# Kernel tuning notes

Measured on AMD Instinct MI355X. Metric: run time of the kernel, lower is better.

Reference implementation:

```python
import jax, jax.numpy as jnp
import numpy as np

B, S, E, H, T = 2, 1024, 1024, 16, 32
D = E // H  # head_dim = 64
EPS = 1e-12
SCALE = float(np.sqrt(T) / np.sqrt(D))  # sqrt(num_templates) * 1/sqrt(head_dim)


def _apply_rope(q, k):
    # q, k: [B, S, H, D] float32 (source casts to float for RoPE)
    d = q.shape[-1]
    s = q.shape[1]
    inv_freq = 1.0 / (10000.0 ** (jnp.arange(0, d, 2, dtype=jnp.float32) / d))
    ang = jnp.arange(s, dtype=jnp.float32)[:, None] * inv_freq[None, :]  # [S, D/2]
    cis = jnp.exp(1j * ang)[None, :, None, :]  # [1, S, 1, D/2] complex64

    def rot(v):
        vc = v.reshape(v.shape[:-1] + (d // 2, 2))
        vc = jax.lax.complex(vc[..., 0], vc[..., 1]) * cis
        return jnp.stack([jnp.real(vc), jnp.imag(vc)], axis=-1).reshape(v.shape)

    return rot(q), rot(k)


def _l2norm(v):
    # F.normalize(v, dim=-1): v / max(||v||, eps)
    n = jnp.sqrt(jnp.sum(v * v, axis=-1, keepdims=True))
    return v / jnp.maximum(n, EPS)


def _forward(x, Wq, Wk, Wv, Wo, templates, bind_proj):
    b, s, e = x.shape
    h, d = H, D
    q = (x @ Wq.T).reshape(b, s, h, d)
    k = (x @ Wk.T).reshape(b, s, h, d)
    v = (x @ Wv.T).reshape(b, s, h, d)
    q, k = _apply_rope(q, k)
    q = q.transpose(0, 2, 1, 3)  # [B,H,S,D]
    k = k.transpose(0, 2, 1, 3)
    v = v.transpose(0, 2, 1, 3)

    tpl = _l2norm(templates)  # [H,T,D]
    # forward rfft uses norm='ortho' in the source
    q_freq = jnp.fft.rfft(q, axis=-1, norm='ortho')  # [B,H,S,F], F=D//2+1
    k_freq = jnp.fft.rfft(k, axis=-1, norm='ortho')
    t_conj = jnp.conj(jnp.fft.rfft(tpl, axis=-1, norm='ortho'))[None, :, None, :, :]  # [1,H,1,T,F]

    # NOTE: irfft in the source uses the DEFAULT 'backward' norm (asymmetric with
    # the ortho rfft) -- reproduce that exactly.
    q_bind = jnp.fft.irfft(q_freq[:, :, :, None, :] * t_conj, n=d, axis=-1)  # [B,H,S,T,D]
    k_bind = jnp.fft.irfft(k_freq[:, :, :, None, :] * t_conj, n=d, axis=-1)

    proj = bind_proj[None, :, None, None, :]  # [1,H,1,1,D]
    q_sig = _l2norm(jnp.sum(q_bind * proj, axis=-1))  # [B,H,S,T]
    k_sig = _l2norm(jnp.sum(k_bind * proj, axis=-1))

    scores = jnp.einsum('bhqt,bhkt->bhqk', q_sig, k_sig) * SCALE  # [B,H,S,S]
    attn = jax.nn.softmax(scores, axis=-1)  # dropout is identity in eval mode
    out = jnp.einsum('bhqk,bhkd->bqhd', attn, v).reshape(b, s, e)
    return out @ Wo.T


def setup_inputs() -> dict:
    key = jax.random.key(0)
    ks = jax.random.split(key, 7)
    lim = 1.0 / np.sqrt(E)
    x = jax.random.normal(ks[0], (B, S, E), jnp.float32)
    Wq = jax.random.uniform(ks[1], (E, E), jnp.float32, -lim, lim)
    Wk = jax.random.uniform(ks[2], (E, E), jnp.float32, -lim, lim)
    Wv = jax.random.uniform(ks[3], (E, E), jnp.float32, -lim, lim)
    Wo = jax.random.uniform(ks[4], (E, E), jnp.float32, -lim, lim)
    templates = jax.random.normal(ks[5], (H, T, D), jnp.float32)
    bind_proj = jax.random.normal(ks[6], (H, D), jnp.float32) * 0.02
    return {"x": x, "Wq": Wq, "Wk": Wk, "Wv": Wv, "Wo": Wo,
            "templates": templates, "bind_proj": bind_proj}


def reference(x, Wq, Wk, Wv, Wo, templates, bind_proj):
    return _forward(x, Wq, Wk, Wv, Wo, templates, bind_proj)
```

## Files before the change

kernel.cpp:

```cpp
#include <hip/hip_runtime.h>
#include <math.h>

#define S_ 1024
#define T_ 32
#define SCALE_F 0.7071067811865476f

typedef unsigned int uint;
typedef unsigned short ushort;
typedef __bf16 bf16x8 __attribute__((ext_vector_type(8)));
typedef float f32x16 __attribute__((ext_vector_type(16)));

union FragU { uint4 q; bf16x8 v; };

#define MFMA(a, b, c) __builtin_amdgcn_mfma_f32_32x32x16_bf16((a), (b), (c), 0, 0, 0)

__device__ __forceinline__ uint rne16(float f) {
  uint u = __builtin_bit_cast(uint, f);
  u += 0x7fffu + ((u >> 16) & 1u);
  return u >> 16;
}

__device__ __forceinline__ void split8a(const float* f, uint4& hi, uint4& lo) {
  uint h[8], m[8];
#pragma unroll
  for (int i = 0; i < 8; ++i) {
    uint u = __builtin_bit_cast(uint, f[i]);
    h[i] = u >> 16;
    float fh = __builtin_bit_cast(float, u & 0xffff0000u);
    m[i] = __builtin_bit_cast(uint, f[i] - fh) >> 16;
  }
  hi = make_uint4(h[0] | (h[1] << 16), h[2] | (h[3] << 16),
                  h[4] | (h[5] << 16), h[6] | (h[7] << 16));
  lo = make_uint4(m[0] | (m[1] << 16), m[2] | (m[3] << 16),
                  m[4] | (m[5] << 16), m[6] | (m[7] << 16));
}

__device__ __forceinline__ uint4 rne8(const float4& A, const float4& B) {
  float f[8] = {A.x, A.y, A.z, A.w, B.x, B.y, B.z, B.w};
  uint h[8];
#pragma unroll
  for (int i = 0; i < 8; ++i) h[i] = rne16(f[i]);
  return make_uint4(h[0] | (h[1] << 16), h[2] | (h[3] << 16),
                    h[4] | (h[5] << 16), h[6] | (h[7] << 16));
}

__global__ __launch_bounds__(256) void k_cvtall(
    const float* __restrict__ X, const float* __restrict__ Wq,
    const float* __restrict__ Wk, const float* __restrict__ Wv,
    const float* __restrict__ Wo, ushort* __restrict__ Xb,
    ushort* __restrict__ Wqb, ushort* __restrict__ Wkb,
    ushort* __restrict__ Wvb, ushort* __restrict__ Wob) {
  int i = blockIdx.x * 256 + threadIdx.x;
  const float* src;
  ushort* dst;
  int j;
  if (i < 262144)      { src = X;  dst = Xb;  j = i; }
  else if (i < 393216) { src = Wq; dst = Wqb; j = i - 262144; }
  else if (i < 524288) { src = Wk; dst = Wkb; j = i - 393216; }
  else if (i < 655360) { src = Wv; dst = Wvb; j = i - 524288; }
  else                 { src = Wo; dst = Wob; j = i - 655360; }
  float4 a = *reinterpret_cast<const float4*>(src + j * 8);
  float4 b = *reinterpret_cast<const float4*>(src + j * 8 + 4);
  *reinterpret_cast<uint4*>(dst + j * 8) = rne8(a, b);
}

__global__ __launch_bounds__(64) void k_cs(float* __restrict__ cs) {
  int s = blockIdx.x * 2 + (threadIdx.x >> 5);
  int p = threadIdx.x & 31;
  float invf = powf(10000.0f, (-2.0f * p) / 64.0f);
  float sn, c;
  sincosf((float)s * invf, &sn, &c);
  cs[s * 64 + 2 * p] = c;
  cs[s * 64 + 2 * p + 1] = sn;
}

__global__ __launch_bounds__(64) void k_prep_A(const float* __restrict__ tpl,
                                               const float* __restrict__ proj,
                                               ushort* __restrict__ Ahh,
                                               ushort* __restrict__ Ahl) {
  int ht = blockIdx.x;
  int h = ht >> 5;
  int lane = threadIdx.x;
  float tv = tpl[ht * 64 + lane];
  float ss = tv * tv;
#pragma unroll
  for (int off = 1; off < 64; off <<= 1) ss += __shfl_xor(ss, off);
  float rn = 1.0f / fmaxf(sqrtf(ss), 1e-12f);
  __shared__ float tn[64];
  tn[lane] = tv * rn;
  __syncthreads();
  float acc = 0.f;
#pragma unroll
  for (int j = 0; j < 64; ++j) acc += proj[h * 64 + j] * tn[(lane - j) & 63];
  float v = acc * 0.125f;
  uint u = __builtin_bit_cast(uint, v);
  uint hi = u >> 16;
  float fh = __builtin_bit_cast(float, u & 0xffff0000u);
  uint lo = __builtin_bit_cast(uint, v - fh) >> 16;
  Ahh[ht * 64 + lane] = (ushort)hi;
  Ahl[ht * 64 + lane] = (ushort)lo;
}

__global__ __launch_bounds__(256) void k_qkv(
    const ushort* __restrict__ Xb,
    const ushort* __restrict__ Wqb, const ushort* __restrict__ Wkb,
    const ushort* __restrict__ Wvb,
    const ushort* __restrict__ Ahh, const ushort* __restrict__ Ahl,
    const float* __restrict__ cs,
    ushort* __restrict__ Qs, ushort* __restrict__ Ks,
    ushort* __restrict__ Vt) {
  __shared__ __align__(16) char smem[34816];

  const int z = blockIdx.z;
  const ushort* Wm = (z == 0) ? Wqb : (z == 1) ? Wkb : Wvb;
  const int m0 = blockIdx.y * 128;
  const int n0 = blockIdx.x * 64;
  const int h = blockIdx.x;

  const int tid = threadIdx.x;
  const int l = tid & 63;
  const int wid = tid >> 6;
  const int wr = wid >> 1, wc = wid & 1;
  const int l31 = l & 31, lhi = l >> 5;

  const int sr = tid >> 2;
  const int sc = tid & 3;

  const int offA0 = (sr) * 64 + ((sc ^ ((sr >> 1) & 3)) << 4);
  const int offA1 = (sr + 64) * 64 + ((sc ^ (((sr + 64) >> 1) & 3)) << 4);
  const int offB = 8192 + sr * 64 + ((sc ^ ((sr >> 1) & 3)) << 4);

  const ushort* apsrc0 = Xb + (size_t)(m0 + sr) * 1024 + sc * 8;
  const ushort* apsrc1 = Xb + (size_t)(m0 + sr + 64) * 1024 + sc * 8;
  const ushort* bpsrc = Wm + (size_t)(n0 + sr) * 1024 + sc * 8;

  f32x16 acc0 = 0.0f, acc1 = 0.0f;

  {
    uint4 a0 = *reinterpret_cast<const uint4*>(apsrc0);
    uint4 a1 = *reinterpret_cast<const uint4*>(apsrc1);
    uint4 b = *reinterpret_cast<const uint4*>(bpsrc);
    *reinterpret_cast<uint4*>(smem + offA0) = a0;
    *reinterpret_cast<uint4*>(smem + offA1) = a1;
    *reinterpret_cast<uint4*>(smem + offB) = b;
  }
  __syncthreads();

  int cur = 0;
  for (int t = 0; t < 32; ++t) {
    const bool more = (t < 31);
    uint4 na0, na1, nb;
    if (more) {
      const int kn = (t + 1) * 32;
      na0 = *reinterpret_cast<const uint4*>(apsrc0 + kn);
      na1 = *reinterpret_cast<const uint4*>(apsrc1 + kn);
      nb = *reinterpret_cast<const uint4*>(bpsrc + kn);
    }

    const char* base = smem + cur * 12288;
#pragma unroll
    for (int kst = 0; kst < 2; ++kst) {
      FragU ah0, ah1, bh;
      {
        int row = wr * 64 + l31;
        int cc = (kst * 2 + lhi) ^ ((row >> 1) & 3);
        ah0.q = *reinterpret_cast<const uint4*>(base + row * 64 + cc * 16);
      }
      {
        int row = wr * 64 + 32 + l31;
        int cc = (kst * 2 + lhi) ^ ((row >> 1) & 3);
        ah1.q = *reinterpret_cast<const uint4*>(base + row * 64 + cc * 16);
      }
      {
        int brow = wc * 32 + l31;
        int bcc = (kst * 2 + lhi) ^ ((brow >> 1) & 3);
        bh.q = *reinterpret_cast<const uint4*>(base + 8192 + brow * 64 + bcc * 16);
      }
      acc0 = MFMA(ah0.v, bh.v, acc0);
      acc1 = MFMA(ah1.v, bh.v, acc1);
    }

    if (more) {
      char* dst = smem + (cur ^ 1) * 12288;
      *reinterpret_cast<uint4*>(dst + offA0) = na0;
      *reinterpret_cast<uint4*>(dst + offA1) = na1;
      *reinterpret_cast<uint4*>(dst + offB) = nb;
      __syncthreads();
      cur ^= 1;
    }
  }

  if (z == 2) {
    int d = wc * 32 + l31;
#pragma unroll
    for (int fm = 0; fm < 2; ++fm) {
      const f32x16& a = fm ? acc1 : acc0;
#pragma unroll
      for (int j = 0; j < 16; ++j) {
        int rl = fm * 32 + (j & 3) + ((j >> 2) & 3) * 8 + 4 * lhi;
        int m = m0 + wr * 64 + rl;
        int b = m >> 10, s = m & 1023;
        Vt[((size_t)((b * 16 + h) * 64 + d)) * 1024 + s] = (ushort)rne16(a[j]);
      }
    }
    return;
  }

  ushort* Sig = (z == 0) ? Qs : Ks;
  float* dmp = reinterpret_cast<float*>(smem);
  __syncthreads();
#pragma unroll
  for (int fm = 0; fm < 2; ++fm) {
    const f32x16& a = fm ? acc1 : acc0;
#pragma unroll
    for (int j = 0; j < 16; ++j) {
      int rl = fm * 32 + (j & 3) + ((j >> 2) & 3) * 8 + 4 * lhi;
      dmp[(wr * 64 + rl) * 68 + wc * 32 + l31] = a[j];
    }
  }
  __syncthreads();

  int srow = wr * 64 + wc * 32 + l31;
  int sq = (m0 + srow) & 1023;
  f32x16 sacc = 0.0f;
#pragma unroll
  for (int kst = 0; kst < 4; ++kst) {
    const float* dp = &dmp[srow * 68 + kst * 16 + lhi * 8];
    float4 x0 = *reinterpret_cast<const float4*>(dp);
    float4 x1 = *reinterpret_cast<const float4*>(dp + 4);
    const float* cp = &cs[sq * 64 + kst * 16 + lhi * 8];
    float4 c0 = *reinterpret_cast<const float4*>(cp);
    float4 c1 = *reinterpret_cast<const float4*>(cp + 4);
    float r[8];
    r[0] = x0.x * c0.x - x0.y * c0.y;
    r[1] = x0.x * c0.y + x0.y * c0.x;
    r[2] = x0.z * c0.z - x0.w * c0.w;
    r[3] = x0.z * c0.w + x0.w * c0.z;
    r[4] = x1.x * c1.x - x1.y * c1.y;
    r[5] = x1.x * c1.y + x1.y * c1.x;
    r[6] = x1.z * c1.z - x1.w * c1.w;
    r[7] = x1.z * c1.w + x1.w * c1.z;
    FragU ah, al;
    split8a(r, ah.q, al.q);
    size_t boff = ((size_t)(h * 32 + l31) * 64 + kst * 16 + lhi * 8);
    FragU bh, bl;
    bh.q = *reinterpret_cast<const uint4*>(Ahh + boff);
    bl.q = *reinterpret_cast<const uint4*>(Ahl + boff);
    sacc = MFMA(al.v, bh.v, sacc);
    sacc = MFMA(ah.v, bl.v, sacc);
    sacc = MFMA(ah.v, bh.v, sacc);
  }
#pragma unroll
  for (int j = 0; j < 16; ++j) {
    float v = sacc[j];
    float ss = v * v;
    ss += __shfl_xor(ss, 1);
    ss += __shfl_xor(ss, 2);
    ss += __shfl_xor(ss, 4);
    ss += __shfl_xor(ss, 8);
    ss += __shfl_xor(ss, 16);
    float rn = 1.0f / fmaxf(sqrtf(ss), 1e-12f);
    int rl = (j & 3) + ((j >> 2) & 3) * 8 + 4 * lhi;
    int m = m0 + wr * 64 + wc * 32 + rl;
    int bb = m >> 10, s2 = m & 1023;
    Sig[(((size_t)(bb * 16 + h)) * 1024 + s2) * 32 + l31] =
        (ushort)rne16(v * rn);
  }
}

__global__ __launch_bounds__(128) void k_attn(const ushort* __restrict__ Qs,
                                              const ushort* __restrict__ Ks,
                                              const ushort* __restrict__ Vt,
                                              ushort* __restrict__ O) {
  __shared__ ushort plds[2][32][68];

  const int tid = threadIdx.x;
  const int l = tid & 63;
  const int wid = tid >> 6;
  const int l31 = l & 31, lhi = l >> 5;
  const int bh = blockIdx.y;
  const int q0 = blockIdx.x * 64 + wid * 32;

  FragU aq0, aq1;
  {
    const ushort* qp = Qs + ((size_t)bh * 1024 + q0 + l31) * 32 + lhi * 8;
    aq0.q = *reinterpret_cast<const uint4*>(qp);
    aq1.q = *reinterpret_cast<const uint4*>(qp + 16);
  }

  const ushort* kbase = Ks + (size_t)bh * 1024 * 32;
  const ushort* vbase = Vt + (size_t)bh * 64 * 1024;

  f32x16 oacc0 = 0.0f, oacc1 = 0.0f;
  float pden[16];
#pragma unroll
  for (int r = 0; r < 16; ++r) pden[r] = 0.f;

  for (int kt = 0; kt < 16; ++kt) {
    const int k0 = kt * 64;
    f32x16 sacc[2];
    sacc[0] = 0.0f;
    sacc[1] = 0.0f;
#pragma unroll
    for (int nt = 0; nt < 2; ++nt) {
      const ushort* kp = kbase + (size_t)(k0 + nt * 32 + l31) * 32 + lhi * 8;
      FragU b0, b1;
      b0.q = *reinterpret_cast<const uint4*>(kp);
      b1.q = *reinterpret_cast<const uint4*>(kp + 16);
      sacc[nt] = MFMA(aq0.v, b0.v, sacc[nt]);
      sacc[nt] = MFMA(aq1.v, b1.v, sacc[nt]);
    }
#pragma unroll
    for (int nt = 0; nt < 2; ++nt) {
#pragma unroll
      for (int r = 0; r < 16; ++r) {
        float e = __expf(sacc[nt][r] * SCALE_F);
        pden[r] += e;
        int q = (r & 3) + ((r >> 2) << 3) + 4 * lhi;
        plds[wid][q][nt * 32 + l31] = (ushort)rne16(e);
      }
    }
    __builtin_amdgcn_wave_barrier();
#pragma unroll
    for (int kst = 0; kst < 4; ++kst) {
      FragU ap;
      const ushort* pp = &plds[wid][l31][kst * 16 + lhi * 8];
      uint2 plo = *reinterpret_cast<const uint2*>(pp);
      uint2 phi = *reinterpret_cast<const uint2*>(pp + 4);
      ap.q = make_uint4(plo.x, plo.y, phi.x, phi.y);
      FragU bv0, bv1;
      const ushort* vp0 = vbase + (size_t)l31 * 1024 + k0 + kst * 16 + lhi * 8;
      bv0.q = *reinterpret_cast<const uint4*>(vp0);
      bv1.q = *reinterpret_cast<const uint4*>(vp0 + 32 * 1024);
      oacc0 = MFMA(ap.v, bv0.v, oacc0);
      oacc1 = MFMA(ap.v, bv1.v, oacc1);
    }
  }

#pragma unroll
  for (int r = 0; r < 16; ++r) {
    float s = pden[r];
    s += __shfl_xor(s, 1);
    s += __shfl_xor(s, 2);
    s += __shfl_xor(s, 4);
    s += __shfl_xor(s, 8);
    s += __shfl_xor(s, 16);
    pden[r] = 1.0f / s;
  }

  const int b = bh >> 4, h = bh & 15;
#pragma unroll
  for (int r = 0; r < 16; ++r) {
    int q = q0 + (r & 3) + ((r >> 2) << 3) + 4 * lhi;
    size_t row = ((size_t)b * 1024 + q) * 1024 + h * 64;
    O[row + l31] = (ushort)rne16(oacc0[r] * pden[r]);
    O[row + 32 + l31] = (ushort)rne16(oacc1[r] * pden[r]);
  }
}

__global__ __launch_bounds__(256) void k_final(const ushort* __restrict__ Xb,
                                               const ushort* __restrict__ Wb,
                                               float* __restrict__ Y) {
  __shared__ __align__(16) char smem[16384];

  const int m0 = blockIdx.y * 64;
  const int n0 = blockIdx.x * 64;
  const int tid = threadIdx.x;
  const int l = tid & 63;
  const int wid = tid >> 6;
  const int wr = wid >> 1, wc = wid & 1;
  const int l31 = l & 31, lhi = l >> 5;
  const int sr = tid >> 2;
  const int sc = tid & 3;

  const int offA = sr * 64 + ((sc ^ ((sr >> 1) & 3)) << 4);
  const int offB = 4096 + offA;
  const ushort* apsrc = Xb + (size_t)(m0 + sr) * 1024 + sc * 8;
  const ushort* bpsrc = Wb + (size_t)(n0 + sr) * 1024 + sc * 8;

  f32x16 acc = 0.0f;

  {
    uint4 av = *reinterpret_cast<const uint4*>(apsrc);
    uint4 bv = *reinterpret_cast<const uint4*>(bpsrc);
    *reinterpret_cast<uint4*>(smem + offA) = av;
    *reinterpret_cast<uint4*>(smem + offB) = bv;
  }
  __syncthreads();

  int cur = 0;
  for (int t = 0; t < 32; ++t) {
    const bool more = (t < 31);
    uint4 na, nb;
    if (more) {
      const int kn = (t + 1) * 32;
      na = *reinterpret_cast<const uint4*>(apsrc + kn);
      nb = *reinterpret_cast<const uint4*>(bpsrc + kn);
    }

    const char* base = smem + cur * 8192;
#pragma unroll
    for (int kst = 0; kst < 2; ++kst) {
      FragU ah, bh;
      int row = wr * 32 + l31;
      int cc = (kst * 2 + lhi) ^ ((row >> 1) & 3);
      ah.q = *reinterpret_cast<const uint4*>(base + row * 64 + cc * 16);
      int brow = wc * 32 + l31;
      int bcc = (kst * 2 + lhi) ^ ((brow >> 1) & 3);
      bh.q = *reinterpret_cast<const uint4*>(base + 4096 + brow * 64 + bcc * 16);
      acc = MFMA(ah.v, bh.v, acc);
    }

    if (more) {
      char* dst = smem + (cur ^ 1) * 8192;
      *reinterpret_cast<uint4*>(dst + offA) = na;
      *reinterpret_cast<uint4*>(dst + offB) = nb;
      __syncthreads();
      cur ^= 1;
    }
  }

#pragma unroll
  for (int j = 0; j < 16; ++j) {
    int rl = (j & 3) + ((j >> 2) & 3) * 8 + 4 * lhi;
    int m = m0 + wr * 32 + rl;
    Y[(size_t)m * 1024 + n0 + wc * 32 + l31] = acc[j];
  }
}

extern "C" void kernel_launch(void* const* d_in, const int* in_sizes, int n_in,
                              void* d_out, int out_size, void* d_ws,
                              size_t ws_size, hipStream_t stream) {
  const float* x = (const float*)d_in[0];
  const float* Wq = (const float*)d_in[1];
  const float* Wk = (const float*)d_in[2];
  const float* Wv = (const float*)d_in[3];
  const float* Wo = (const float*)d_in[4];
  const float* tpl = (const float*)d_in[5];
  const float* proj = (const float*)d_in[6];
  float* out = (float*)d_out;

  char* ws = (char*)d_ws;
  size_t off = 0;
  auto alloc = [&](size_t bytes) {
    void* p = ws + off;
    off += (bytes + 255) & ~(size_t)255;
    return p;
  };

  const size_t MB = 1024 * 1024;
  bool big = ws_size >= 22 * MB;

  ushort *Xb, *Wvb, *obuf;
  float* cs;
  ushort *Ahh, *Ahl, *Wqb, *Wkb, *Wob, *qs, *ks, *vt;

  if (big) {
    Xb = (ushort*)alloc(4 * MB);
    cs = (float*)alloc((size_t)1024 * 64 * 4);
    Ahh = (ushort*)alloc((size_t)16 * 32 * 64 * 2);
    Ahl = (ushort*)alloc((size_t)16 * 32 * 64 * 2);
    Wqb = (ushort*)alloc(2 * MB);
    Wkb = (ushort*)alloc(2 * MB);
    Wvb = (ushort*)alloc(2 * MB);
    Wob = (ushort*)alloc(2 * MB);
    qs = (ushort*)alloc(2 * MB);
    ks = (ushort*)alloc(2 * MB);
    vt = (ushort*)alloc(4 * MB);
    obuf = Xb;
  } else {
    cs = (float*)alloc((size_t)1024 * 64 * 4);
    Ahh = (ushort*)alloc((size_t)16 * 32 * 64 * 2);
    Ahl = (ushort*)alloc((size_t)16 * 32 * 64 * 2);
    Wqb = (ushort*)alloc(2 * MB);
    Wkb = (ushort*)alloc(2 * MB);
    Wob = (ushort*)alloc(2 * MB);
    qs = (ushort*)alloc(2 * MB);
    ks = (ushort*)alloc(2 * MB);
    vt = (ushort*)alloc(4 * MB);
    obuf = (ushort*)ws;
    Xb = (ushort*)d_out;
    Wvb = (ushort*)((char*)d_out + 4 * MB);
  }

  k_cvtall<<<dim3(3072), dim3(256), 0, stream>>>(x, Wq, Wk, Wv, Wo, Xb, Wqb,
                                                 Wkb, Wvb, Wob);
  k_cs<<<dim3(512), dim3(64), 0, stream>>>(cs);
  k_prep_A<<<dim3(512), dim3(64), 0, stream>>>(tpl, proj, Ahh, Ahl);
  k_qkv<<<dim3(16, 16, 3), dim3(256), 0, stream>>>(Xb, Wqb, Wkb, Wvb, Ahh, Ahl,
                                                   cs, qs, ks, vt);
  k_attn<<<dim3(16, 32), dim3(128), 0, stream>>>(qs, ks, vt, obuf);
  k_final<<<dim3(16, 32), dim3(256), 0, stream>>>(obuf, Wob, out);
}
```

Measured before the change: 100.7 us.

## Split attention over key dimension with partial sums and reduction kernel

Splits the attention kernel across four key chunks using a third grid dimension. Each chunk writes unnormalized fp32 partial outputs and denominators to a large workspace buffer, and a new reduction kernel sums them and normalizes. This targets low occupancy: the original grid had only 512 blocks of 128 threads, which cannot fill the GPU. In exchange it adds a 32 MB fp32 partial-output round trip and an extra launch. The split path is used only when the workspace is at least 64 MB; otherwise the original monolithic kernel runs. No max subtraction is done, which relies on the scores being bounded, as in the original.

New measurement: 95.47 us. -5.2%, faster.

```diff
diff --git a/kernel.cpp b/kernel.cpp
--- a/kernel.cpp
+++ b/kernel.cpp
@@ -271,7 +271,8 @@
 __global__ __launch_bounds__(128) void k_attn(const ushort* __restrict__ Qs,
                                               const ushort* __restrict__ Ks,
                                               const ushort* __restrict__ Vt,
-                                              ushort* __restrict__ O) {
+                                              float* __restrict__ Po,
+                                              float* __restrict__ Pd) {
   __shared__ ushort plds[2][32][68];
 
   const int tid = threadIdx.x;
@@ -279,6 +280,7 @@
   const int wid = tid >> 6;
   const int l31 = l & 31, lhi = l >> 5;
   const int bh = blockIdx.y;
+  const int z = blockIdx.z;
   const int q0 = blockIdx.x * 64 + wid * 32;
 
   FragU aq0, aq1;
@@ -296,7 +298,7 @@
 #pragma unroll
   for (int r = 0; r < 16; ++r) pden[r] = 0.f;
 
-  for (int kt = 0; kt < 16; ++kt) {
+  for (int kt = z * 4; kt < z * 4 + 4; ++kt) {
     const int k0 = kt * 64;
     f32x16 sacc[2];
     sacc[0] = 0.0f;
@@ -345,6 +347,114 @@
     s += __shfl_xor(s, 4);
     s += __shfl_xor(s, 8);
     s += __shfl_xor(s, 16);
+    pden[r] = s;
+  }
+
+  const size_t zb = (size_t)z * 32 + bh;
+#pragma unroll
+  for (int r = 0; r < 16; ++r) {
+    int q = q0 + (r & 3) + ((r >> 2) << 3) + 4 * lhi;
+    size_t row = zb * 1024 + q;
+    Po[row * 64 + l31] = oacc0[r];
+    Po[row * 64 + 32 + l31] = oacc1[r];
+    if (l31 == 0) Pd[row] = pden[r];
+  }
+}
+
+__global__ __launch_bounds__(256) void k_attnred(const float* __restrict__ Po,
+                                                 const float* __restrict__ Pd,
+                                                 ushort* __restrict__ O) {
+  int idx = blockIdx.x * 4 + (threadIdx.x >> 6);
+  int d = threadIdx.x & 63;
+  float den = 0.f, val = 0.f;
+#pragma unroll
+  for (int zc = 0; zc < 4; ++zc) {
+    size_t row = (size_t)zc * 32768 + idx;
+    den += Pd[row];
+    val += Po[row * 64 + d];
+  }
+  int bh = idx >> 10, q = idx & 1023;
+  int b = bh >> 4, h = bh & 15;
+  O[((size_t)(b * 1024 + q)) * 1024 + h * 64 + d] = (ushort)rne16(val / den);
+}
+
+__global__ __launch_bounds__(128) void k_attn_mono(const ushort* __restrict__ Qs,
+                                                   const ushort* __restrict__ Ks,
+                                                   const ushort* __restrict__ Vt,
+                                                   ushort* __restrict__ O) {
+  __shared__ ushort plds[2][32][68];
+
+  const int tid = threadIdx.x;
+  const int l = tid & 63;
+  const int wid = tid >> 6;
+  const int l31 = l & 31, lhi = l >> 5;
+  const int bh = blockIdx.y;
+  const int q0 = blockIdx.x * 64 + wid * 32;
+
+  FragU aq0, aq1;
+  {
+    const ushort* qp = Qs + ((size_t)bh * 1024 + q0 + l31) * 32 + lhi * 8;
+    aq0.q = *reinterpret_cast<const uint4*>(qp);
+    aq1.q = *reinterpret_cast<const uint4*>(qp + 16);
+  }
+
+  const ushort* kbase = Ks + (size_t)bh * 1024 * 32;
+  const ushort* vbase = Vt + (size_t)bh * 64 * 1024;
+
+  f32x16 oacc0 = 0.0f, oacc1 = 0.0f;
+  float pden[16];
+#pragma unroll
+  for (int r = 0; r < 16; ++r) pden[r] = 0.f;
+
+  for (int kt = 0; kt < 16; ++kt) {
+    const int k0 = kt * 64;
+    f32x16 sacc[2];
+    sacc[0] = 0.0f;
+    sacc[1] = 0.0f;
+#pragma unroll
+    for (int nt = 0; nt < 2; ++nt) {
+      const ushort* kp = kbase + (size_t)(k0 + nt * 32 + l31) * 32 + lhi * 8;
+      FragU b0, b1;
+      b0.q = *reinterpret_cast<const uint4*>(kp);
+      b1.q = *reinterpret_cast<const uint4*>(kp + 16);
+      sacc[nt] = MFMA(aq0.v, b0.v, sacc[nt]);
+      sacc[nt] = MFMA(aq1.v, b1.v, sacc[nt]);
+    }
+#pragma unroll
+    for (int nt = 0; nt < 2; ++nt) {
+#pragma unroll
+      for (int r = 0; r < 16; ++r) {
+        float e = __expf(sacc[nt][r] * SCALE_F);
+        pden[r] += e;
+        int q = (r & 3) + ((r >> 2) << 3) + 4 * lhi;
+        plds[wid][q][nt * 32 + l31] = (ushort)rne16(e);
+      }
+    }
+    __builtin_amdgcn_wave_barrier();
+#pragma unroll
+    for (int kst = 0; kst < 4; ++kst) {
+      FragU ap;
+      const ushort* pp = &plds[wid][l31][kst * 16 + lhi * 8];
+      uint2 plo = *reinterpret_cast<const uint2*>(pp);
+      uint2 phi = *reinterpret_cast<const uint2*>(pp + 4);
+      ap.q = make_uint4(plo.x, plo.y, phi.x, phi.y);
+      FragU bv0, bv1;
+      const ushort* vp0 = vbase + (size_t)l31 * 1024 + k0 + kst * 16 + lhi * 8;
+      bv0.q = *reinterpret_cast<const uint4*>(vp0);
+      bv1.q = *reinterpret_cast<const uint4*>(vp0 + 32 * 1024);
+      oacc0 = MFMA(ap.v, bv0.v, oacc0);
+      oacc1 = MFMA(ap.v, bv1.v, oacc1);
+    }
+  }
+
+#pragma unroll
+  for (int r = 0; r < 16; ++r) {
+    float s = pden[r];
+    s += __shfl_xor(s, 1);
+    s += __shfl_xor(s, 2);
+    s += __shfl_xor(s, 4);
+    s += __shfl_xor(s, 8);
+    s += __shfl_xor(s, 16);
     pden[r] = 1.0f / s;
   }
 
@@ -449,13 +559,15 @@
   };
 
   const size_t MB = 1024 * 1024;
+  bool huge = ws_size >= 64 * MB;
   bool big = ws_size >= 22 * MB;
 
   ushort *Xb, *Wvb, *obuf;
   float* cs;
   ushort *Ahh, *Ahl, *Wqb, *Wkb, *Wob, *qs, *ks, *vt;
-
-  if (big) {
+  float *Po = nullptr, *Pd = nullptr;
+
+  if (big || huge) {
     Xb = (ushort*)alloc(4 * MB);
     cs = (float*)alloc((size_t)1024 * 64 * 4);
     Ahh = (ushort*)alloc((size_t)16 * 32 * 64 * 2);
@@ -467,6 +579,10 @@
     qs = (ushort*)alloc(2 * MB);
     ks = (ushort*)alloc(2 * MB);
     vt = (ushort*)alloc(4 * MB);
+    if (huge) {
+      Po = (float*)alloc(32 * MB);
+      Pd = (float*)alloc((size_t)4 * 32768 * 4);
+    }
     obuf = Xb;
   } else {
     cs = (float*)alloc((size_t)1024 * 64 * 4);
@@ -489,6 +605,11 @@
   k_prep_A<<<dim3(512), dim3(64), 0, stream>>>(tpl, proj, Ahh, Ahl);
   k_qkv<<<dim3(16, 16, 3), dim3(256), 0, stream>>>(Xb, Wqb, Wkb, Wvb, Ahh, Ahl,
                                                    cs, qs, ks, vt);
-  k_attn<<<dim3(16, 32), dim3(128), 0, stream>>>(qs, ks, vt, obuf);
+  if (huge) {
+    k_attn<<<dim3(16, 32, 4), dim3(128), 0, stream>>>(qs, ks, vt, Po, Pd);
+    k_attnred<<<dim3(8192), dim3(256), 0, stream>>>(Po, Pd, obuf);
+  } else {
+    k_attn_mono<<<dim3(16, 32), dim3(128), 0, stream>>>(qs, ks, vt, obuf);
+  }
   k_final<<<dim3(16, 32), dim3(256), 0, stream>>>(obuf, Wob, out);
 }
```
